# Performance work log

Measured on AMD Instinct MI355X. Metric: run time of the kernel, lower is better.

## Reference

```python
import jax, jax.numpy as jnp
import numpy as np

N_USERS, N_ITEMS, D, E = 60000, 40000, 64, 1600000
N = N_USERS + N_ITEMS


def setup_inputs() -> dict:
    key = jax.random.key(0)
    ks = jax.random.split(key, 7)
    user_embedding = jax.random.normal(ks[0], (N_USERS, D), dtype=jnp.float32)
    item_embedding = jax.random.normal(ks[1], (N_ITEMS, D), dtype=jnp.float32)
    # per-node symmetric-normalization scalar (e.g. 1/sqrt(deg)), positive
    norm = jax.random.uniform(ks[2], (N, 1), dtype=jnp.float32, minval=0.01, maxval=1.0)
    src = jax.random.randint(ks[3], (E,), 0, N, dtype=jnp.int32)
    dst = jax.random.randint(ks[4], (E,), 0, N, dtype=jnp.int32)
    # xavier-uniform linear weights, stored as [out_dim, in_dim] like nn.Linear
    limit = float(np.sqrt(6.0 / (D + D)))
    W1 = jax.random.uniform(ks[5], (D, D), dtype=jnp.float32, minval=-limit, maxval=limit)
    W2 = jax.random.uniform(ks[6], (D, D), dtype=jnp.float32, minval=-limit, maxval=limit)
    return {"user_embedding": user_embedding, "item_embedding": item_embedding,
            "norm": norm, "src": src, "dst": dst, "W1": W1, "W2": W2}


def reference(user_embedding, item_embedding, norm, src, dst, W1, W2):
    h = jnp.concatenate([user_embedding, item_embedding], axis=0)  # [N, D]
    # W1(h) can be computed once per node, then gathered per edge.
    h1 = h @ W1.T                                                  # [N, D]
    hs = h[src]                                                    # [E, D] gather
    hd = h[dst]                                                    # [E, D] gather
    # message: W1(h_src) + W2(h_src * h_dst), scaled by norm_src * norm_dst
    msg = (h1[src] + (hs * hd) @ W2.T) * (norm[src] * norm[dst])   # [E, D]
    m = jax.ops.segment_sum(msg, dst, num_segments=h.shape[0])     # scatter-sum -> [N, D]
    m = m + h1
    out = jnp.where(m >= 0, m, 0.2 * m)  # LeakyReLU(0.2); dropout=0 (eval) is identity
    # F.normalize(p=2, dim=1), eps=1e-12
    l2 = jnp.sqrt(jnp.sum(out * out, axis=1, keepdims=True))
    return out / jnp.maximum(l2, 1e-12)
```

## Files before the change

kernel.cpp:

```cpp
#include <hip/hip_runtime.h>

#define DD 64

typedef __attribute__((ext_vector_type(8))) short bfrag;
typedef __attribute__((ext_vector_type(4))) float ffrag;

static __device__ __forceinline__ short f2bf(float f) {
  union { float f; unsigned u; } v; v.f = f;
  unsigned r = v.u + 0x7fff + ((v.u >> 16) & 1);
  return (short)(r >> 16);
}
static __device__ __forceinline__ float bf2f(unsigned short u) {
  union { unsigned u; float f; } v; v.u = ((unsigned)u) << 16; return v.f;
}


__global__ void chist_kernel(const int* __restrict__ dst, int* __restrict__ ccnt,
                             int E, int NB) {
  __shared__ int ch[512];
  for (int i = threadIdx.x; i < 512; i += 256) ch[i] = 0;
  __syncthreads();
  int ebase = blockIdx.x * 4096;
#pragma unroll
  for (int j = 0; j < 16; ++j) {
    int e = ebase + j * 256 + threadIdx.x;
    if (e < E) atomicAdd(&ch[dst[e] >> 8], 1);
  }
  __syncthreads();
  for (int b = threadIdx.x; b < NB; b += 256) {
    int c = ch[b];
    if (c) atomicAdd(&ccnt[b], c);
  }
}

__global__ void cscan_kernel(const int* __restrict__ ccnt, int* __restrict__ cbase,
                             int* __restrict__ ccursor, int NB) {
  __shared__ int wtot[4];
  int t = threadIdx.x;
  int i0 = t * 2, i1 = t * 2 + 1;
  int v0 = (i0 < NB) ? ccnt[i0] : 0;
  int v1 = (i1 < NB) ? ccnt[i1] : 0;
  int s = v0 + v1;
  int lane = t & 63, w = t >> 6;
  int ps = s;
#pragma unroll
  for (int off = 1; off < 64; off <<= 1) {
    int tmp = __shfl_up(ps, off);
    if (lane >= off) ps += tmp;
  }
  if (lane == 63) wtot[w] = ps;
  __syncthreads();
  int wbase = 0;
  for (int k = 0; k < w; ++k) wbase += wtot[k];
  int excl = wbase + ps - s;
  if (i0 < NB) { cbase[i0] = excl;      ccursor[i0] = excl; }
  if (i1 < NB) { cbase[i1] = excl + v0; ccursor[i1] = excl + v0; }
  if (t == 0) {
    int tot = 0;
    for (int k = 0; k < 4; ++k) tot += wtot[k];
    cbase[NB] = tot;
  }
}

__global__ void cscatter_kernel(const int* __restrict__ src, const int* __restrict__ dst,
                                int* __restrict__ ccursor, unsigned* __restrict__ pairb,
                                int E, int NB) {
  __shared__ int bh[512], bbase[512], brank[512];
  for (int i = threadIdx.x; i < 512; i += 256) { bh[i] = 0; brank[i] = 0; }
  __syncthreads();
  int ebase = blockIdx.x * 4096;
  int se[16], de[16];
#pragma unroll
  for (int j = 0; j < 16; ++j) {
    int e = ebase + j * 256 + threadIdx.x;
    if (e < E) {
      se[j] = src[e];
      de[j] = dst[e];
      atomicAdd(&bh[de[j] >> 8], 1);
    } else {
      se[j] = -1; de[j] = 0;
    }
  }
  __syncthreads();
  for (int b = threadIdx.x; b < NB; b += 256) {
    int c = bh[b];
    bbase[b] = c ? atomicAdd(&ccursor[b], c) : 0;
  }
  __syncthreads();
#pragma unroll
  for (int j = 0; j < 16; ++j) {
    if (se[j] >= 0) {
      int b = de[j] >> 8;
      int r = atomicAdd(&brank[b], 1);
      pairb[bbase[b] + r] = ((unsigned)se[j] << 8) | (unsigned)(de[j] & 255);
    }
  }
}

__global__ void fine_kernel(const unsigned* __restrict__ pairb,
                            const int* __restrict__ cbase,
                            int* __restrict__ offs, int* __restrict__ cnt,
                            int* __restrict__ ebuf, int Nn) {
  __shared__ int fh[256], fcur[256];
  __shared__ int wtot[4];
  int t = threadIdx.x, b = blockIdx.x;
  int nb0 = b << 8;
  int cbeg = cbase[b], cend = cbase[b + 1];
  fh[t] = 0;
  __syncthreads();
  for (int p = cbeg + t; p < cend; p += 256) atomicAdd(&fh[pairb[p] & 255u], 1);
  __syncthreads();
  int val = fh[t];
  int lane = t & 63, w = t >> 6;
  int ps = val;
#pragma unroll
  for (int off = 1; off < 64; off <<= 1) {
    int tmp = __shfl_up(ps, off);
    if (lane >= off) ps += tmp;
  }
  if (lane == 63) wtot[w] = ps;
  __syncthreads();
  int wbase = 0;
  for (int k = 0; k < w; ++k) wbase += wtot[k];
  int excl = wbase + ps - val;
  int node = nb0 + t;
  if (node < Nn) { offs[node] = cbeg + excl; cnt[node] = val; }
  fcur[t] = cbeg + excl;
  __syncthreads();
  for (int p = cbeg + t; p < cend; p += 256) {
    unsigned v = pairb[p];
    int pos = atomicAdd(&fcur[v & 255u], 1);
    ebuf[pos] = (int)(v >> 8);
  }
}


__global__ void hconv_kernel(const float* __restrict__ ue, const float* __restrict__ ie,
                             const float* __restrict__ norm,
                             unsigned short* __restrict__ hsc, int Nn, int NU) {
  int tid = blockIdx.x * blockDim.x + threadIdx.x;
  if (tid >= Nn * 16) return;
  int row = tid >> 4;
  int q = tid & 15;
  const float* hr = (row < NU) ? ue + (size_t)row * DD : ie + (size_t)(row - NU) * DD;
  float nr = norm[row];
  float4 hv = reinterpret_cast<const float4*>(hr)[q];
  unsigned u0 = (unsigned short)f2bf(nr * hv.x);
  unsigned u1 = (unsigned short)f2bf(nr * hv.y);
  unsigned u2 = (unsigned short)f2bf(nr * hv.z);
  unsigned u3 = (unsigned short)f2bf(nr * hv.w);
  uint2 pk;
  pk.x = u0 | (u1 << 16);
  pk.y = u2 | (u3 << 16);
  *reinterpret_cast<uint2*>(hsc + (size_t)row * DD + q * 4) = pk;
}


__launch_bounds__(256)
__global__ void gather_hsc_kernel(const unsigned short* __restrict__ hsc,
                                  const int* __restrict__ offs,
                                  const int* __restrict__ cnt,
                                  const int* __restrict__ ebuf,
                                  float* __restrict__ g, int Nn) {
  int lane = threadIdx.x & 63;
  int wid = blockIdx.x * 4 + (threadIdx.x >> 6);
  int d = __builtin_amdgcn_readfirstlane(wid);
  if (d >= Nn) return;
  int beg = __builtin_amdgcn_readfirstlane(offs[d]);
  int num = __builtin_amdgcn_readfirstlane(cnt[d]);
  float a0 = 0.f, a1 = 0.f, a2 = 0.f, a3 = 0.f;
  int i = 0;
  for (; i + 4 <= num; i += 4) {
    int s0 = ebuf[beg + i + 0];
    int s1 = ebuf[beg + i + 1];
    int s2 = ebuf[beg + i + 2];
    int s3 = ebuf[beg + i + 3];
    a0 += bf2f(hsc[(size_t)s0 * DD + lane]);
    a1 += bf2f(hsc[(size_t)s1 * DD + lane]);
    a2 += bf2f(hsc[(size_t)s2 * DD + lane]);
    a3 += bf2f(hsc[(size_t)s3 * DD + lane]);
  }
  for (; i < num; ++i) a0 += bf2f(hsc[(size_t)ebuf[beg + i] * DD + lane]);
  g[(size_t)d * DD + lane] = (a0 + a1) + (a2 + a3);
}


__launch_bounds__(256)
__global__ void node_mfma_kernel(const float* __restrict__ ue,
                                 const float* __restrict__ ie,
                                 const float* __restrict__ norm,
                                 const float* __restrict__ W1,
                                 const float* __restrict__ W2,
                                 const float* __restrict__ g,
                                 float* __restrict__ out,
                                 int Nn, int NU) {
  int lane = threadIdx.x & 63;
  int l15 = lane & 15;
  int lg  = lane >> 4;
  int tile = blockIdx.x * 4 + (threadIdx.x >> 6);

  bfrag w1f[2][4], w2f[2][4];
#pragma unroll
  for (int jt = 0; jt < 4; ++jt) {
    int wrow = jt * 16 + l15;
#pragma unroll
    for (int ks = 0; ks < 2; ++ks) {
      int kb = ks * 32 + lg * 8;
      const float* p1 = W1 + wrow * DD + kb;
      const float* p2 = W2 + wrow * DD + kb;
#pragma unroll
      for (int j = 0; j < 8; ++j) {
        w1f[ks][jt][j] = f2bf(p1[j]);
        w2f[ks][jt][j] = f2bf(p2[j]);
      }
    }
  }

  if (tile * 16 >= Nn) return;
  int node = tile * 16 + l15;
  int nclamp = (node < Nn) ? node : (Nn - 1);
  const float* hrow = (nclamp < NU) ? ue + (size_t)nclamp * DD
                                    : ie + (size_t)(nclamp - NU) * DD;
  const float* grow = g + (size_t)nclamp * DD;
  float nd = norm[nclamp];

  ffrag acc[4];
#pragma unroll
  for (int jt = 0; jt < 4; ++jt) acc[jt] = (ffrag){0.f, 0.f, 0.f, 0.f};

#pragma unroll
  for (int ks = 0; ks < 2; ++ks) {
    int kb = ks * 32 + lg * 8;
    bfrag xf, yf;
#pragma unroll
    for (int j = 0; j < 8; ++j) {
      float gv = grow[kb + j];
      float hv = hrow[kb + j];
      xf[j] = f2bf(fmaf(nd, gv, hv));
      yf[j] = f2bf(nd * gv * hv);
    }
#pragma unroll
    for (int jt = 0; jt < 4; ++jt) {
      acc[jt] = __builtin_amdgcn_mfma_f32_16x16x32_bf16(xf, w1f[ks][jt], acc[jt], 0, 0, 0);
      acc[jt] = __builtin_amdgcn_mfma_f32_16x16x32_bf16(yf, w2f[ks][jt], acc[jt], 0, 0, 0);
    }
  }

  float v[4][4];
  float ss[4];
#pragma unroll
  for (int r = 0; r < 4; ++r) {
    float s = 0.f;
#pragma unroll
    for (int jt = 0; jt < 4; ++jt) {
      float m = acc[jt][r];
      float t = (m >= 0.f) ? m : 0.2f * m;
      v[r][jt] = t;
      s = fmaf(t, t, s);
    }
#pragma unroll
    for (int off = 1; off < 16; off <<= 1) s += __shfl_xor(s, off);
    ss[r] = s;
  }
#pragma unroll
  for (int r = 0; r < 4; ++r) {
    int orow = tile * 16 + lg * 4 + r;
    if (orow < Nn) {
      float inv = 1.0f / fmaxf(sqrtf(ss[r]), 1e-12f);
#pragma unroll
      for (int jt = 0; jt < 4; ++jt)
        out[(size_t)orow * DD + jt * 16 + l15] = v[r][jt] * inv;
    }
  }
}


__global__ void hist_kernel(const int* __restrict__ dst, int* __restrict__ cnt, int E) {
  int e = blockIdx.x * blockDim.x + threadIdx.x;
  if (e < E) atomicAdd(&cnt[dst[e]], 1);
}

__global__ void scanA_kernel(const int* __restrict__ cnt, int* __restrict__ offs,
                             int* __restrict__ bsum, int Nn) {
  __shared__ int wsum[4];
  int base = blockIdx.x * 4096 + threadIdx.x * 16;
  int v[16];
  int s = 0;
#pragma unroll
  for (int i = 0; i < 16; ++i) {
    int idx = base + i;
    v[i] = (idx < Nn) ? cnt[idx] : 0;
    s += v[i];
  }
  int lane = threadIdx.x & 63, w = threadIdx.x >> 6;
  int ps = s;
#pragma unroll
  for (int off = 1; off < 64; off <<= 1) {
    int t = __shfl_up(ps, off);
    if (lane >= off) ps += t;
  }
  if (lane == 63) wsum[w] = ps;
  __syncthreads();
  int wbase = 0;
  for (int i = 0; i < w; ++i) wbase += wsum[i];
  int texcl = wbase + ps - s;
  int run = texcl;
#pragma unroll
  for (int i = 0; i < 16; ++i) {
    int idx = base + i;
    if (idx < Nn) offs[idx] = run;
    run += v[i];
  }
  if (threadIdx.x == blockDim.x - 1) bsum[blockIdx.x] = texcl + s;
}

__global__ void scanB_kernel(int* __restrict__ bsum, int nb) {
  if (threadIdx.x == 0 && blockIdx.x == 0) {
    int run = 0;
    for (int i = 0; i < nb; ++i) { int t = bsum[i]; bsum[i] = run; run += t; }
  }
}

__global__ void scanC_kernel(int* __restrict__ offs, int* __restrict__ cursor,
                             const int* __restrict__ bsum, int Nn) {
  int i = blockIdx.x * blockDim.x + threadIdx.x;
  if (i < Nn) {
    int v = offs[i] + bsum[i >> 12];
    offs[i] = v;
    cursor[i] = v;
  }
}

__global__ void bucket_kernel(const int* __restrict__ src, const int* __restrict__ dst,
                              int* __restrict__ cursor, int* __restrict__ ebuf, int E) {
  int e = blockIdx.x * blockDim.x + threadIdx.x;
  if (e < E) {
    int d = dst[e];
    int p = atomicAdd(&cursor[d], 1);
    ebuf[p] = src[e];
  }
}

__launch_bounds__(256)
__global__ void gather_g_kernel(const float* __restrict__ ue,
                                const float* __restrict__ ie,
                                const float* __restrict__ norm,
                                const int* __restrict__ offs,
                                const int* __restrict__ cnt,
                                const int* __restrict__ ebuf,
                                float* __restrict__ g,
                                int Nn, int NU) {
  int lane = threadIdx.x & 63;
  int wid = blockIdx.x * (blockDim.x >> 6) + (threadIdx.x >> 6);
  int d = __builtin_amdgcn_readfirstlane(wid);
  if (d >= Nn) return;
  int beg = __builtin_amdgcn_readfirstlane(offs[d]);
  int num = __builtin_amdgcn_readfirstlane(cnt[d]);
  float a0 = 0.f, a1 = 0.f, a2 = 0.f, a3 = 0.f;
  int i = 0;
  for (; i + 4 <= num; i += 4) {
    int s0 = ebuf[beg + i + 0];
    int s1 = ebuf[beg + i + 1];
    int s2 = ebuf[beg + i + 2];
    int s3 = ebuf[beg + i + 3];
    float w0 = norm[s0], w1 = norm[s1], w2 = norm[s2], w3 = norm[s3];
    const float* r0 = (s0 < NU) ? ue + (size_t)s0 * DD : ie + (size_t)(s0 - NU) * DD;
    const float* r1 = (s1 < NU) ? ue + (size_t)s1 * DD : ie + (size_t)(s1 - NU) * DD;
    const float* r2 = (s2 < NU) ? ue + (size_t)s2 * DD : ie + (size_t)(s2 - NU) * DD;
    const float* r3 = (s3 < NU) ? ue + (size_t)s3 * DD : ie + (size_t)(s3 - NU) * DD;
    a0 = fmaf(w0, r0[lane], a0);
    a1 = fmaf(w1, r1[lane], a1);
    a2 = fmaf(w2, r2[lane], a2);
    a3 = fmaf(w3, r3[lane], a3);
  }
  for (; i < num; ++i) {
    int s0 = ebuf[beg + i];
    float w0 = norm[s0];
    const float* r0 = (s0 < NU) ? ue + (size_t)s0 * DD : ie + (size_t)(s0 - NU) * DD;
    a0 = fmaf(w0, r0[lane], a0);
  }
  g[(size_t)d * DD + lane] = (a0 + a1) + (a2 + a3);
}


extern "C" void kernel_launch(void* const* d_in, const int* in_sizes, int n_in,
                              void* d_out, int out_size, void* d_ws, size_t ws_size,
                              hipStream_t stream) {
  const float* ue   = (const float*)d_in[0];
  const float* ie   = (const float*)d_in[1];
  const float* norm = (const float*)d_in[2];
  const int*   src  = (const int*)d_in[3];
  const int*   dst  = (const int*)d_in[4];
  const float* W1   = (const float*)d_in[5];
  const float* W2   = (const float*)d_in[6];
  float* out = (float*)d_out;

  int NU = in_sizes[0] / DD;
  int Nn = in_sizes[2];
  int E  = in_sizes[3];

  int NB = (Nn + 255) >> 8;

  size_t un = ((size_t)E > (size_t)Nn * 32) ? (size_t)E : (size_t)Nn * 32;
  size_t new_ints = 1538 + 2 * (size_t)Nn + (size_t)E + un + 4;
  size_t new_bytes = new_ints * sizeof(int);

  size_t csr_ints = (size_t)3 * Nn + 64 + (size_t)E;
  size_t csr_bytes = csr_ints * sizeof(int);

  if (NB <= 512 && ws_size >= new_bytes) {
    int* ccnt    = (int*)d_ws;
    int* cbase   = ccnt + 512;
    int* ccursor = cbase + 513;
    int* offs    = ccnt + 1538;
    int* cnt     = offs + Nn;
    int* ebuf    = cnt + Nn;
    uintptr_t up = (uintptr_t)(ebuf + E);
    up = (up + 7) & ~(uintptr_t)7;
    unsigned*       pairb = (unsigned*)up;
    unsigned short* hsc   = (unsigned short*)up;
    float* g = out;

    hipMemsetAsync(ccnt, 0, 512 * sizeof(int), stream);

    int EB = (E + 4095) / 4096;
    chist_kernel<<<EB, 256, 0, stream>>>(dst, ccnt, E, NB);
    cscan_kernel<<<1, 256, 0, stream>>>(ccnt, cbase, ccursor, NB);
    cscatter_kernel<<<EB, 256, 0, stream>>>(src, dst, ccursor, pairb, E, NB);
    fine_kernel<<<NB, 256, 0, stream>>>(pairb, cbase, offs, cnt, ebuf, Nn);
    hconv_kernel<<<(Nn * 16 + 255) / 256, 256, 0, stream>>>(ue, ie, norm, hsc, Nn, NU);
    gather_hsc_kernel<<<(Nn + 3) / 4, 256, 0, stream>>>(hsc, offs, cnt, ebuf, g, Nn);

    int ntiles = (Nn + 15) / 16;
    node_mfma_kernel<<<(ntiles + 3) / 4, 256, 0, stream>>>(ue, ie, norm, W1, W2, g, out,
                                                           Nn, NU);
  } else if (ws_size >= csr_bytes) {
    int* cnt    = (int*)d_ws;
    int* offs   = cnt + Nn;
    int* cursor = offs + Nn;
    int* bsum   = cursor + Nn;
    int* ebuf   = bsum + 64;
    size_t g_bytes = (size_t)Nn * DD * sizeof(float);
    float* g = (ws_size >= csr_bytes + g_bytes) ? (float*)(ebuf + E) : out;

    hipMemsetAsync(cnt, 0, (size_t)Nn * sizeof(int), stream);
    int eblk = (E + 255) / 256;
    hist_kernel<<<eblk, 256, 0, stream>>>(dst, cnt, E);
    int nblkA = (Nn + 4095) / 4096;
    scanA_kernel<<<nblkA, 256, 0, stream>>>(cnt, offs, bsum, Nn);
    scanB_kernel<<<1, 64, 0, stream>>>(bsum, nblkA);
    scanC_kernel<<<(Nn + 255) / 256, 256, 0, stream>>>(offs, cursor, bsum, Nn);
    bucket_kernel<<<eblk, 256, 0, stream>>>(src, dst, cursor, ebuf, E);
    gather_g_kernel<<<(Nn + 3) / 4, 256, 0, stream>>>(ue, ie, norm, offs, cnt, ebuf,
                                                      g, Nn, NU);
    int ntiles = (Nn + 15) / 16;
    node_mfma_kernel<<<(ntiles + 3) / 4, 256, 0, stream>>>(ue, ie, norm, W1, W2, g, out,
                                                           Nn, NU);
  }
}
```

Baseline: 156.3 us.

## Fuse neighbor gather with MFMA node transform via shared-memory tile

Merges the per-node gather kernel with the per-tile MFMA transform kernel. Each wave gathers the aggregates for its 16 nodes into LDS and then runs the W1/W2 bf16 MFMAs, LeakyReLU and L2 normalization directly. This removes the fp32 intermediate g round trip through global memory and one kernel launch. It also reconstructs h from the bf16 scaled copy instead of the fp32 inputs, which lowers precision. The exchange is far less parallelism in the gather phase, since a wave now walks 16 nodes serially instead of one wave per node, and this may hurt latency hiding for the random accesses.

```diff
diff --git a/kernel.cpp b/kernel.cpp
--- a/kernel.cpp
+++ b/kernel.cpp
@@ -155,33 +155,131 @@
   *reinterpret_cast<uint2*>(hsc + (size_t)row * DD + q * 4) = pk;
 }
 
-
 __launch_bounds__(256)
-__global__ void gather_hsc_kernel(const unsigned short* __restrict__ hsc,
-                                  const int* __restrict__ offs,
-                                  const int* __restrict__ cnt,
-                                  const int* __restrict__ ebuf,
-                                  float* __restrict__ g, int Nn) {
+__global__ void gather_mfma_kernel(const unsigned short* __restrict__ hsc,
+                                   const float* __restrict__ norm,
+                                   const float* __restrict__ W1,
+                                   const float* __restrict__ W2,
+                                   const int* __restrict__ offs,
+                                   const int* __restrict__ cnt,
+                                   const int* __restrict__ ebuf,
+                                   float* __restrict__ out, int Nn) {
+  __shared__ float gt[4][16][68];
   int lane = threadIdx.x & 63;
-  int wid = blockIdx.x * 4 + (threadIdx.x >> 6);
-  int d = __builtin_amdgcn_readfirstlane(wid);
-  if (d >= Nn) return;
-  int beg = __builtin_amdgcn_readfirstlane(offs[d]);
-  int num = __builtin_amdgcn_readfirstlane(cnt[d]);
-  float a0 = 0.f, a1 = 0.f, a2 = 0.f, a3 = 0.f;
-  int i = 0;
-  for (; i + 4 <= num; i += 4) {
-    int s0 = ebuf[beg + i + 0];
-    int s1 = ebuf[beg + i + 1];
-    int s2 = ebuf[beg + i + 2];
-    int s3 = ebuf[beg + i + 3];
-    a0 += bf2f(hsc[(size_t)s0 * DD + lane]);
-    a1 += bf2f(hsc[(size_t)s1 * DD + lane]);
-    a2 += bf2f(hsc[(size_t)s2 * DD + lane]);
-    a3 += bf2f(hsc[(size_t)s3 * DD + lane]);
-  }
-  for (; i < num; ++i) a0 += bf2f(hsc[(size_t)ebuf[beg + i] * DD + lane]);
-  g[(size_t)d * DD + lane] = (a0 + a1) + (a2 + a3);
+  int w = threadIdx.x >> 6;
+  int tile = blockIdx.x * 4 + w;
+  if (tile * 16 >= Nn) return;
+
+  for (int n = 0; n < 16; ++n) {
+    int node = tile * 16 + n;
+    float a0 = 0.f, a1 = 0.f, a2 = 0.f, a3 = 0.f;
+    if (node < Nn) {
+      int beg = __builtin_amdgcn_readfirstlane(offs[node]);
+      int num = __builtin_amdgcn_readfirstlane(cnt[node]);
+      int i = 0;
+      for (; i + 8 <= num; i += 8) {
+        int s0 = ebuf[beg + i + 0];
+        int s1 = ebuf[beg + i + 1];
+        int s2 = ebuf[beg + i + 2];
+        int s3 = ebuf[beg + i + 3];
+        int s4 = ebuf[beg + i + 4];
+        int s5 = ebuf[beg + i + 5];
+        int s6 = ebuf[beg + i + 6];
+        int s7 = ebuf[beg + i + 7];
+        float v0 = bf2f(hsc[(size_t)s0 * DD + lane]);
+        float v1 = bf2f(hsc[(size_t)s1 * DD + lane]);
+        float v2 = bf2f(hsc[(size_t)s2 * DD + lane]);
+        float v3 = bf2f(hsc[(size_t)s3 * DD + lane]);
+        float v4 = bf2f(hsc[(size_t)s4 * DD + lane]);
+        float v5 = bf2f(hsc[(size_t)s5 * DD + lane]);
+        float v6 = bf2f(hsc[(size_t)s6 * DD + lane]);
+        float v7 = bf2f(hsc[(size_t)s7 * DD + lane]);
+        a0 += v0 + v4;
+        a1 += v1 + v5;
+        a2 += v2 + v6;
+        a3 += v3 + v7;
+      }
+      for (; i < num; ++i) a0 += bf2f(hsc[(size_t)ebuf[beg + i] * DD + lane]);
+    }
+    gt[w][n][lane] = (a0 + a1) + (a2 + a3);
+  }
+  __builtin_amdgcn_sched_barrier(0);
+
+  int l15 = lane & 15;
+  int lg  = lane >> 4;
+  bfrag w1f[2][4], w2f[2][4];
+#pragma unroll
+  for (int jt = 0; jt < 4; ++jt) {
+    int wrow = jt * 16 + l15;
+#pragma unroll
+    for (int ks = 0; ks < 2; ++ks) {
+      int kb = ks * 32 + lg * 8;
+      const float* p1 = W1 + wrow * DD + kb;
+      const float* p2 = W2 + wrow * DD + kb;
+#pragma unroll
+      for (int j = 0; j < 8; ++j) {
+        w1f[ks][jt][j] = f2bf(p1[j]);
+        w2f[ks][jt][j] = f2bf(p2[j]);
+      }
+    }
+  }
+
+  int node = tile * 16 + l15;
+  int nclamp = (node < Nn) ? node : (Nn - 1);
+  float nd = norm[nclamp];
+  float rnd = 1.0f / nd;
+
+  ffrag acc[4];
+#pragma unroll
+  for (int jt = 0; jt < 4; ++jt) acc[jt] = (ffrag){0.f, 0.f, 0.f, 0.f};
+
+#pragma unroll
+  for (int ks = 0; ks < 2; ++ks) {
+    int kb = ks * 32 + lg * 8;
+    float4 g0 = *reinterpret_cast<const float4*>(&gt[w][l15][kb]);
+    float4 g1 = *reinterpret_cast<const float4*>(&gt[w][l15][kb + 4]);
+    bfrag hb = *reinterpret_cast<const bfrag*>(hsc + (size_t)nclamp * DD + kb);
+    float gv[8] = {g0.x, g0.y, g0.z, g0.w, g1.x, g1.y, g1.z, g1.w};
+    bfrag xf, yf;
+#pragma unroll
+    for (int j = 0; j < 8; ++j) {
+      float hj = bf2f((unsigned short)hb[j]);
+      xf[j] = f2bf(fmaf(nd, gv[j], hj * rnd));
+      yf[j] = f2bf(gv[j] * hj);
+    }
+#pragma unroll
+    for (int jt = 0; jt < 4; ++jt) {
+      acc[jt] = __builtin_amdgcn_mfma_f32_16x16x32_bf16(xf, w1f[ks][jt], acc[jt], 0, 0, 0);
+      acc[jt] = __builtin_amdgcn_mfma_f32_16x16x32_bf16(yf, w2f[ks][jt], acc[jt], 0, 0, 0);
+    }
+  }
+
+  float v[4][4];
+  float ss[4];
+#pragma unroll
+  for (int r = 0; r < 4; ++r) {
+    float s = 0.f;
+#pragma unroll
+    for (int jt = 0; jt < 4; ++jt) {
+      float m = acc[jt][r];
+      float t = (m >= 0.f) ? m : 0.2f * m;
+      v[r][jt] = t;
+      s = fmaf(t, t, s);
+    }
+#pragma unroll
+    for (int off = 1; off < 16; off <<= 1) s += __shfl_xor(s, off);
+    ss[r] = s;
+  }
+#pragma unroll
+  for (int r = 0; r < 4; ++r) {
+    int orow = tile * 16 + lg * 4 + r;
+    if (orow < Nn) {
+      float inv = 1.0f / fmaxf(sqrtf(ss[r]), 1e-12f);
+#pragma unroll
+      for (int jt = 0; jt < 4; ++jt)
+        out[(size_t)orow * DD + jt * 16 + l15] = v[r][jt] * inv;
+    }
+  }
 }
 
 
@@ -419,7 +517,6 @@
     up = (up + 7) & ~(uintptr_t)7;
     unsigned*       pairb = (unsigned*)up;
     unsigned short* hsc   = (unsigned short*)up;
-    float* g = out;
 
     hipMemsetAsync(ccnt, 0, 512 * sizeof(int), stream);
 
@@ -429,11 +526,10 @@
     cscatter_kernel<<<EB, 256, 0, stream>>>(src, dst, ccursor, pairb, E, NB);
     fine_kernel<<<NB, 256, 0, stream>>>(pairb, cbase, offs, cnt, ebuf, Nn);
     hconv_kernel<<<(Nn * 16 + 255) / 256, 256, 0, stream>>>(ue, ie, norm, hsc, Nn, NU);
-    gather_hsc_kernel<<<(Nn + 3) / 4, 256, 0, stream>>>(hsc, offs, cnt, ebuf, g, Nn);
 
     int ntiles = (Nn + 15) / 16;
-    node_mfma_kernel<<<(ntiles + 3) / 4, 256, 0, stream>>>(ue, ie, norm, W1, W2, g, out,
-                                                           Nn, NU);
+    gather_mfma_kernel<<<(ntiles + 3) / 4, 256, 0, stream>>>(hsc, norm, W1, W2,
+                                                             offs, cnt, ebuf, out, Nn);
   } else if (ws_size >= csr_bytes) {
     int* cnt    = (int*)d_ws;
     int* offs   = cnt + Nn;
```

Measured after the change: 173.9 us. 11.3% more time.
